# Performance work log

Measured on AMD Instinct MI355X. Metric: run time of the kernel, lower is better.

The kernel has to match this reference:

```python
import jax, jax.numpy as jnp
import numpy as np
from jax import lax

NEG = -1e30  # log-space 'zero' that stays finite for stable grads

T, B, V, L = 2000, 64, 128, 100


def ctc_cost(acts, labels2d, sizes, label_lens):
    """warp-ctc style CTC: acts are raw logits (T,B,V), blank index 0.
    Returns summed negative log-likelihood over the batch, shape (1,)."""
    Tn, Bn, Vn = acts.shape
    Ln = labels2d.shape[1]
    S = 2 * Ln + 1  # extended label length: blank,l1,blank,l2,...,blank
    lp = jax.nn.log_softmax(acts, axis=-1)  # (T,B,V)

    # extended label sequence per example: even positions blank(0), odd = labels
    ext = jnp.zeros((Bn, S), dtype=labels2d.dtype).at[:, 1::2].set(labels2d)
    # skip (s-2 -> s) allowed iff ext[s] != blank and ext[s] != ext[s-2]
    prev2 = jnp.concatenate([jnp.full((Bn, 2), -1, ext.dtype), ext[:, :-2]], axis=1)
    can_skip = (ext != 0) & (ext != prev2)  # (B,S)

    # gather per-state emission log-probs for all timesteps: (T,B,S)
    lp_ext = jnp.take_along_axis(lp, jnp.broadcast_to(ext[None], (Tn, Bn, S)), axis=2)

    # alpha init at t=0: states 0 (blank) and 1 (first label)
    alpha0 = (jnp.full((Bn, S), NEG, lp.dtype)
              .at[:, 0].set(lp_ext[0, :, 0])
              .at[:, 1].set(lp_ext[0, :, 1]))

    # per-timestep activity mask: freeze alpha once t >= sizes[b]
    active = jnp.arange(1, Tn)[:, None] < sizes[None, :]  # (T-1, B)

    def step(alpha, x):
        lp_t, act = x  # (B,S), (B,)
        a1 = jnp.concatenate([jnp.full((Bn, 1), NEG, alpha.dtype), alpha[:, :-1]], axis=1)
        a2 = jnp.concatenate([jnp.full((Bn, 2), NEG, alpha.dtype), alpha[:, :-2]], axis=1)
        a2 = jnp.where(can_skip, a2, NEG)
        new = jnp.logaddexp(jnp.logaddexp(alpha, a1), a2) + lp_t
        alpha = jnp.where(act[:, None], new, alpha)
        return alpha, None

    alpha, _ = lax.scan(step, alpha0, (lp_ext[1:], active))

    # log-likelihood ends at extended states S_b-1 (final blank) and S_b-2 (final label)
    S_b = 2 * label_lens + 1
    last = jnp.take_along_axis(alpha, (S_b - 1)[:, None], axis=1)[:, 0]
    last2 = jnp.take_along_axis(alpha, (S_b - 2)[:, None], axis=1)[:, 0]
    ll = jnp.logaddexp(last, last2)  # (B,)
    return -jnp.sum(ll)[None]  # shape (1,) like the torch module


def setup_inputs() -> dict:
    key = jax.random.key(0)
    k1, k2, k3 = jax.random.split(key, 3)
    inp = jax.random.normal(k1, (T, B, V), dtype=jnp.float32)
    # labels in [1, V): 0 is reserved for blank
    target = jax.random.randint(k2, (B * L,), 1, V, dtype=jnp.int32)
    # frame counts in [T//2, T], always >= 2L+1 so every path is feasible
    sizes = jax.random.randint(k3, (B,), T // 2, T + 1, dtype=jnp.int32)
    label_lens = jnp.full((B,), L, dtype=jnp.int32)
    return {"input": inp, "target": target, "sizes": sizes, "label_lens": label_lens}


def reference(input, target, sizes, label_lens):
    labels2d = target.reshape(sizes.shape[0], -1)  # all label_lens equal -> clean reshape
    return ctc_cost(input, labels2d, sizes, label_lens)
```

## Files before the change

kernel.cpp:

```cpp
#include <hip/hip_runtime.h>


#define TT 2000
#define BB 64
#define VV 128
#define LL 100
#define REC 104
#define REC_BASE 256
#define NEGF (-1e30f)
#define L2E 1.44269504f
#define LN2 0.69314718f

#define SB_STATE (REC_BASE + BB * TT * REC)
#define AREA 336

__device__ __forceinline__ float wave_max64(float v) {
#pragma unroll
  for (int o = 32; o > 0; o >>= 1) v = fmaxf(v, __shfl_xor(v, o, 64));
  return v;
}
__device__ __forceinline__ float wave_sum64(float v) {
#pragma unroll
  for (int o = 32; o > 0; o >>= 1) v += __shfl_xor(v, o, 64);
  return v;
}

__global__ __launch_bounds__(256) void k_gather(const float* __restrict__ acts,
                                                const int* __restrict__ target,
                                                float* __restrict__ ws) {
  const int lane = threadIdx.x & 63;
  const int w = threadIdx.x >> 6;
  const int r = blockIdx.x * 4 + w;
  if (r >= TT * BB) return;
  const int b = r % BB;
  const int t = r / BB;
  const float* row = acts + (size_t)r * VV;
  float x0 = row[lane];
  float x1 = row[lane + 64];
  float m = wave_max64(fmaxf(x0, x1));
  float e = __builtin_exp2f((x0 - m) * L2E) + __builtin_exp2f((x1 - m) * L2E);
  float s = wave_sum64(e);
  float lse = m + __builtin_log2f(s) * LN2;
  const int* lab = target + b * LL;
  int c1 = lab[lane];
  int j2 = 64 + lane;
  int c2 = (j2 < LL) ? lab[j2] : 1;
  float y1lo = __shfl(x0, c1 & 63, 64);
  float y1hi = __shfl(x1, c1 & 63, 64);
  float y1 = (c1 < 64) ? y1lo : y1hi;
  float y2lo = __shfl(x0, c2 & 63, 64);
  float y2hi = __shfl(x1, c2 & 63, 64);
  float y2 = (c2 < 64) ? y2lo : y2hi;
  float g1 = y1 - lse;
  float g2 = (j2 < LL) ? (y2 - lse) : NEGF;
  float gb = __shfl(x0, 0, 64) - lse;
  float gm = wave_max64(fmaxf(fmaxf(g1, g2), gb));
  float q1 = __builtin_exp2f((g1 - gm) * L2E);
  float q2 = (j2 < LL) ? __builtin_exp2f((g2 - gm) * L2E) : 0.0f;
  float* rec = ws + REC_BASE + ((size_t)b * TT + t) * REC;
  rec[2 + lane] = q1;
  if (lane < 38) rec[66 + lane] = q2;
  if (lane == 0) { rec[0] = __builtin_exp2f((gb - gm) * L2E); rec[1] = gm; }
}

#define BPER __builtin_amdgcn_ds_bpermute

#define DECLR(P) float2 P##h0, P##h1, P##h2, P##h3; \
                 float4 P##q0, P##q1, P##q2, P##q3; float P##aY

#define PREF(P, bidx) do {                                                   \
  int bi_ = (bidx); bi_ = (bi_ < bcap) ? bi_ : bcap; if (bi_ < 0) bi_ = 0;   \
  const float* r0_ = recs_b + (size_t)(tA + TS * 4 * bi_) * REC;             \
  P##h0 = *(const float2*)(r0_);                                             \
  P##h1 = *(const float2*)(r0_ + TS * REC);                                  \
  P##h2 = *(const float2*)(r0_ + TS * 2 * REC);                              \
  P##h3 = *(const float2*)(r0_ + TS * 3 * REC);                              \
  float2 lo0_ = *(const float2*)(r0_ + vofs);                                \
  float2 hi0_ = *(const float2*)(r0_ + vofs + 2);                            \
  float2 lo1_ = *(const float2*)(r0_ + TS * REC + vofs);                     \
  float2 hi1_ = *(const float2*)(r0_ + TS * REC + vofs + 2);                 \
  float2 lo2_ = *(const float2*)(r0_ + TS * 2 * REC + vofs);                 \
  float2 hi2_ = *(const float2*)(r0_ + TS * 2 * REC + vofs + 2);             \
  float2 lo3_ = *(const float2*)(r0_ + TS * 3 * REC + vofs);                 \
  float2 hi3_ = *(const float2*)(r0_ + TS * 3 * REC + vofs + 2);             \
  P##aY = r0_[ayofs];                                                        \
  if constexpr (DIR) {                                                       \
    P##q0 = (float4){hi0_.y, hi0_.x, lo0_.y * cmask, lo0_.x * cmask};        \
    P##q1 = (float4){hi1_.y, hi1_.x, lo1_.y * cmask, lo1_.x * cmask};        \
    P##q2 = (float4){hi2_.y, hi2_.x, lo2_.y * cmask, lo2_.x * cmask};        \
    P##q3 = (float4){hi3_.y, hi3_.x, lo3_.y * cmask, lo3_.x * cmask};        \
  } else {                                                                   \
    P##q0 = (float4){lo0_.x, lo0_.y, hi0_.x, hi0_.y};                        \
    P##q1 = (float4){lo1_.x, lo1_.y, hi1_.x, hi1_.y};                        \
    P##q2 = (float4){lo2_.x, lo2_.y, hi2_.x, hi2_.y};                        \
    P##q3 = (float4){lo3_.x, lo3_.y, hi3_.x, hi3_.y};                        \
  }                                                                          \
} while (0)

#define STEP(qbv, gmv, cx, cy, bx, by, ay, NH) do {                          \
  const float qb_ = (qbv); msum += (gmv);                                    \
  o3 = __builtin_fmaf(cs_o3, o1, o3 + o2) * (cy);                            \
  o2 = (o2 + o1) * qb_;                                                      \
  o1 = __builtin_fmaf(cs_o1, h1, o1 + o0) * (cx);                            \
  o0 = (o0 + h1) * qb_;                                                      \
  if (NH >= 1) { h1 = __builtin_fmaf(cs_h1, h3, h1 + h2) * (by);             \
                 h2 = (h2 + h3) * qb_; }                                     \
  if (NH >= 2) { h3 = __builtin_fmaf(cs_h3, h5, h3 + h4) * (bx);             \
                 h4 = (h4 + h5) * qb_; }                                     \
  if (NH >= 3) { h5 = __builtin_fmaf(cs_h5, h7, h5 + h6) * (ay);             \
                 h6 = (h6 + h7) * qb_; }                                     \
} while (0)

#define COMPA(P) do {                                                        \
  STEP(P##h0.x, P##h0.y, P##q0.z, P##q0.w, P##q0.x, P##q0.y, P##aY, 3);      \
  STEP(P##h1.x, P##h1.y, P##q1.z, P##q1.w, P##q1.x, P##q1.y, 0.f, 2);        \
  STEP(P##h2.x, P##h2.y, P##q2.z, P##q2.w, P##q2.x, P##q2.y, 0.f, 1);        \
  STEP(P##h3.x, P##h3.y, P##q3.z, P##q3.w, 0.f, 0.f, 0.f, 0);                \
  *(float4*)(exb + 4 * l) = (float4){o0, o1, o2, o3};                        \
  ((int*)exb)[256 + l] = offs;                                               \
} while (0)

#define FINL() do {                                                          \
  asm volatile("" ::: "memory");                                             \
  float4 L1_ = *(const float4*)(exb + 4 * ((l >= 1) ? (l - 1) : 0));         \
  float4 L2_ = *(const float4*)(exb + 4 * ((l >= 2) ? (l - 2) : 0));         \
  int ro1_ = ((const int*)exb)[256 + ((l >= 1) ? (l - 1) : 0)];              \
  int ro2_ = ((const int*)exb)[256 + ((l >= 2) ? (l - 2) : 0)];              \
  ro1_ = (l >= 1) ? ro1_ : -(1 << 29);                                       \
  ro2_ = (l >= 2) ? ro2_ : -(1 << 29);                                       \
  float m_ = fmaxf(fmaxf(o0, o1), fmaxf(o2, o3));                            \
  int eb_ = (int)((__float_as_uint(m_) >> 23) & 255u);                       \
  int t1_ = offs + (eb_ ? (eb_ - 127) : -126);                               \
  int mx_ = (ro1_ > ro2_) ? ro1_ : ro2_;                                     \
  int onew_ = (t1_ > mx_) ? t1_ : mx_;                                       \
  int ds_ = offs - onew_;  ds_ = (ds_ < -300) ? -300 : ds_;                  \
  int d1_ = ro1_ - onew_, d2_ = ro2_ - onew_;                                \
  d1_ = (d1_ < -300) ? -300 : d1_;                                           \
  d2_ = (d2_ < -300) ? -300 : d2_;                                           \
  o0 = ldexpf(o0, ds_); o1 = ldexpf(o1, ds_);                                \
  o2 = ldexpf(o2, ds_); o3 = ldexpf(o3, ds_);                                \
  h1 = ldexpf(L1_.w, d1_) * msk1;                                            \
  h2 = ldexpf(L1_.z, d1_) * msk2;                                            \
  h3 = ldexpf(L1_.y, d1_) * msk3;                                            \
  h4 = ldexpf(L1_.x, d1_) * msk4;                                            \
  h5 = ldexpf(L2_.w, d2_) * msk5;                                            \
  h6 = ldexpf(L2_.z, d2_) * msk6;                                            \
  h7 = ldexpf(L2_.y, d2_) * msk7;                                            \
  offs = onew_;                                                              \
} while (0)

template <int DIR>
__device__ __forceinline__ void run_chain(const int* __restrict__ target,
                                          const int* __restrict__ lablens,
                                          const float* __restrict__ recs_b,
                                          float* exb, int size, int b, int l,
                                          float* __restrict__ ws) {
  const int mid = (size - 1) >> 1;
  const int sizeP = DIR ? (size - 1 - mid) : (mid + 1);
  const int* lab = target + b * LL;
  const int lc = (l < 50) ? l : 50;
  const int vofs = DIR ? (100 - 2 * lc) : (2 * lc);
  const int tA = DIR ? (size - 2) : 1;
  constexpr int TS = DIR ? -1 : 1;
  const int bcap = DIR ? ((size - 5) >> 2) : 498;
  int ay_ = DIR ? (104 - 2 * l) : (2 * l - 1);
  ay_ = (ay_ < 0) ? 0 : ((ay_ > 103) ? 103 : ay_);
  const int ayofs = ay_;
  const float cmask = (l < 50) ? 1.f : 0.f;
  const int idx1 = ((l + 63) & 63) << 2;
  const float msk1 = (4 * l - 1 >= 0) ? 1.f : 0.f;
  const float msk2 = (4 * l - 2 >= 0) ? 1.f : 0.f;
  const float msk3 = (4 * l - 3 >= 0) ? 1.f : 0.f;
  const float msk4 = (4 * l - 4 >= 0) ? 1.f : 0.f;
  const float msk5 = (4 * l - 5 >= 0) ? 1.f : 0.f;
  const float msk6 = (4 * l - 6 >= 0) ? 1.f : 0.f;
  const float msk7 = (4 * l - 7 >= 0) ? 1.f : 0.f;
  int i0, i1, i2, i3, i4, i5;
  if constexpr (DIR == 0) { i0 = 2*l+1; i1 = 2*l; i2 = 2*l-1; i3 = 2*l-2; i4 = 2*l-3; i5 = 2*l-4; }
  else { i0 = 98-2*l; i1 = 99-2*l; i2 = 100-2*l; i3 = 101-2*l; i4 = 102-2*l; i5 = 103-2*l; }
#define CLM(x) ((x) < 0 ? 0 : ((x) > 99 ? 99 : (x)))
  const int La = lab[CLM(i0)], Lb_ = lab[CLM(i1)], Lc = lab[CLM(i2)];
  const int Ld = lab[CLM(i3)], Le = lab[CLM(i4)], Lf = lab[CLM(i5)];
  const float cs_o3 = (La != Lb_) ? 1.f : 0.f;
  const float cs_o1 = (Lb_ != Lc) ? 1.f : 0.f;
  const float cs_h1 = (Lc != Ld) ? 1.f : 0.f;
  const float cs_h3 = (Ld != Le) ? 1.f : 0.f;
  const float cs_h5 = (Le != Lf) ? 1.f : 0.f;
  float o0 = 0.f, o1 = 0.f, o2 = 0.f, o3 = 0.f;
  float h1 = 0.f, h2 = 0.f, h3 = 0.f, h4 = 0.f, h5 = 0.f, h6 = 0.f, h7 = 0.f;
  int offs = 0;
  float msum;
  if constexpr (DIR == 0) {
    msum = recs_b[1];
    if (l == 0) { o0 = recs_b[0]; o1 = recs_b[2]; }
    if (l == 1) { h3 = recs_b[2]; h4 = recs_b[0]; }
    if (l == 2) { h7 = recs_b[2]; }
  } else {
    const float* recL = recs_b + (size_t)(size - 1) * REC;
    msum = recL[1];
    const int Lbv = lablens[b];
    const int r0v = 200 - 2 * Lbv;
    auto gi = [&](int rho) -> float {
      if (rho != r0v && rho != r0v + 1) return 0.f;
      if ((rho & 1) == 0) return recL[0];
      return recL[2 + 99 - ((rho - 1) >> 1)];
    };
    o0 = gi(4*l); o1 = gi(4*l+1); o2 = gi(4*l+2); o3 = gi(4*l+3);
    h1 = gi(4*l-1); h2 = gi(4*l-2); h3 = gi(4*l-3); h4 = gi(4*l-4);
    h5 = gi(4*l-5); h6 = gi(4*l-6); h7 = gi(4*l-7);
  }

  const int nb = (sizeP - 1) >> 2;
  DECLR(A); DECLR(B); DECLR(C); DECLR(D);
  PREF(A, 0); PREF(B, 1); PREF(C, 2);
  int blk = 0;
  for (; blk + 4 <= nb; blk += 4) {
    COMPA(A); PREF(D, blk + 3); FINL();
    COMPA(B); PREF(A, blk + 4); FINL();
    COMPA(C); PREF(B, blk + 5); FINL();
    COMPA(D); PREF(C, blk + 6); FINL();
  }
  if (nb - blk >= 1) { COMPA(A); FINL(); }
  if (nb - blk >= 2) { COMPA(B); FINL(); }
  if (nb - blk >= 3) { COMPA(C); FINL(); }
  {
    int rno1 = BPER(idx1, offs);
    int dtl = rno1 - offs;
    dtl = (dtl > 120) ? 120 : ((dtl < -300) ? -300 : dtl);
    for (int tau = 1 + 4 * nb; tau < sizeP; ++tau) {
      const float* rt = recs_b + (size_t)(DIR ? (size - 1 - tau) : tau) * REC;
      float2 hh = *(const float2*)rt;
      float cx, cy;
      if constexpr (DIR == 0) {
        float2 qc = *(const float2*)(rt + 2 + 2 * lc);
        cx = qc.x; cy = qc.y;
      } else {
        float2 qc = *(const float2*)(rt + vofs + 2);
        cx = qc.y * cmask; cy = qc.x * cmask;
      }
      int rp = BPER(idx1, __float_as_int(o3));
      float p = ldexpf(__int_as_float(rp), dtl) * msk1;
      msum += hh.y;
      o3 = __builtin_fmaf(cs_o3, o1, o3 + o2) * cy;
      o2 = (o2 + o1) * hh.x;
      o1 = __builtin_fmaf(cs_o1, p, o1 + o0) * cx;
      o0 = (o0 + p) * hh.x;
    }
    if constexpr (DIR == 0) {
      int rp = BPER(idx1, __float_as_int(o3));
      float p = ldexpf(__int_as_float(rp), dtl) * msk1;
      o3 = __builtin_fmaf(cs_o3, o1, o3 + o2);
      o2 = o2 + o1;
      o1 = __builtin_fmaf(cs_o1, p, o1 + o0);
      o0 = o0 + p;
    }
  }
  float* da = ws + SB_STATE + (size_t)(2 * b + DIR) * AREA;
  ((float4*)da)[l] = (float4){o0, o1, o2, o3};
  ((int*)da)[256 + l] = offs;
  if (l == 0) da[320] = msum;
}

__global__ __launch_bounds__(128, 1) void k_alpha(const int* __restrict__ target,
                                                  const int* __restrict__ sizes,
                                                  const int* __restrict__ lablens,
                                                  float* __restrict__ ws) {
  __shared__ float ldsA[2 * 384];
  const int b = blockIdx.x;
  const int dirw = threadIdx.x >> 6;
  const int l = threadIdx.x & 63;
  float* exb = ldsA + dirw * 384;
  const int size = sizes[b];
  const float* recs_b = ws + REC_BASE + (size_t)b * TT * REC;
  if (dirw == 0) run_chain<0>(target, lablens, recs_b, exb, size, b, l, ws);
  else           run_chain<1>(target, lablens, recs_b, exb, size, b, l, ws);
}

__global__ __launch_bounds__(64) void k_comb(float* __restrict__ ws) {
  const int b = blockIdx.x;
  const int l = threadIdx.x;
  const float* fa = ws + SB_STATE + (size_t)(2 * b) * AREA;
  const float* ba = fa + AREA;
  float4 av = ((const float4*)fa)[l];
  int eF = ((const int*)fa)[256 + l];
  float msF = fa[320], msB = ba[320];
  float pr0, pr1, pr2, pr3; int ex0, ex1, ex2, ex3, sb0, sb1, sb2, sb3;
#define CMP(k, AV, PR, EX, SBE) do {                                         \
    int s_ = 4 * l + (k);                                                    \
    int rho_ = 200 - s_;                                                     \
    int rc_ = (rho_ < 0) ? 0 : rho_;                                         \
    float g_ = ba[rc_];                                                      \
    int eB_ = ((const int*)ba)[256 + (rc_ >> 2)];                            \
    float p_ = (AV) * g_;                                                    \
    bool ok_ = (rho_ >= 0) && (p_ > 0.f);                                    \
    int eb_ = (int)((__float_as_uint(p_) >> 23) & 255u);                     \
    SBE = eF + eB_;                                                          \
    EX = ok_ ? (SBE + (eb_ ? eb_ - 127 : -140)) : (int)0xC0000000;           \
    PR = ok_ ? p_ : 0.f;                                                     \
  } while (0)
  CMP(0, av.x, pr0, ex0, sb0);
  CMP(1, av.y, pr1, ex1, sb1);
  CMP(2, av.z, pr2, ex2, sb2);
  CMP(3, av.w, pr3, ex3, sb3);
  int Em = ex0 > ex1 ? ex0 : ex1;
  Em = ex2 > Em ? ex2 : Em;
  Em = ex3 > Em ? ex3 : Em;
#pragma unroll
  for (int o = 32; o > 0; o >>= 1) {
    int t = __shfl_xor(Em, o, 64);
    Em = (t > Em) ? t : Em;
  }
  float v = 0.f;
#define ACC(PR, SBE) do { if (PR > 0.f) {                                    \
    int sh_ = SBE - Em; sh_ = sh_ < -300 ? -300 : (sh_ > 300 ? 300 : sh_);   \
    v += ldexpf(PR, sh_); } } while (0)
  ACC(pr0, sb0); ACC(pr1, sb1); ACC(pr2, sb2); ACC(pr3, sb3);
  float S = wave_sum64(v);
  if (l == 0) ws[b] = msF + msB + LN2 * ((float)Em + __builtin_log2f(S));
}

__global__ __launch_bounds__(64) void k_final(const float* __restrict__ ws, float* __restrict__ out) {
  float v = (threadIdx.x < BB) ? ws[threadIdx.x] : 0.0f;
  v = wave_sum64(v);
  if (threadIdx.x == 0) out[0] = -v;
}

extern "C" void kernel_launch(void* const* d_in, const int* in_sizes, int n_in,
                              void* d_out, int out_size, void* d_ws, size_t ws_size,
                              hipStream_t stream) {
  const float* acts  = (const float*)d_in[0];
  const int* target  = (const int*)d_in[1];
  const int* sizes   = (const int*)d_in[2];
  const int* lablens = (const int*)d_in[3];
  float* ws  = (float*)d_ws;
  float* out = (float*)d_out;
  const int nrec = TT * BB;
  k_gather<<<dim3(nrec / 4), dim3(256), 0, stream>>>(acts, target, ws);
  k_alpha<<<dim3(BB), dim3(128), 0, stream>>>(target, sizes, lablens, ws);
  k_comb<<<dim3(BB), dim3(64), 0, stream>>>(ws);
  k_final<<<dim3(1), dim3(64), 0, stream>>>(ws, out);
}
```

Before: 131.2 us.

## Store per-step emission ratios as packed bf16 and shorten the prefetch pipeline

The gather kernel now writes the per-label emission ratios as round-to-nearest bf16 pairs packed into 32-bit words, which shrinks each record from 104 to 56 floats. The alpha chain loads one packed word per timestep for its two states and unpacks with shifts and masks. This cuts workspace traffic in both the gather write and the latency-bound recurrence reads. The software prefetch ring also drops from four buffered blocks to three, trading prefetch depth for fewer live registers. The risk is lost precision in the CTC likelihood, since bf16 emission factors are multiplied over up to 2000 steps.

Result: faster. 124.5 us (-5.1%).

```diff
diff --git a/kernel.cpp b/kernel.cpp
--- a/kernel.cpp
+++ b/kernel.cpp
@@ -5,13 +5,13 @@
 #define BB 64
 #define VV 128
 #define LL 100
-#define REC 104
+#define RECW 56
 #define REC_BASE 256
 #define NEGF (-1e30f)
 #define L2E 1.44269504f
 #define LN2 0.69314718f
 
-#define SB_STATE (REC_BASE + BB * TT * REC)
+#define SB_STATE (REC_BASE + BB * TT * RECW)
 #define AREA 336
 
 __device__ __forceinline__ float wave_max64(float v) {
@@ -23,6 +23,12 @@
 #pragma unroll
   for (int o = 32; o > 0; o >>= 1) v += __shfl_xor(v, o, 64);
   return v;
+}
+__device__ __forceinline__ float blo(unsigned u) { return __uint_as_float(u << 16); }
+__device__ __forceinline__ float bhi(unsigned u) { return __uint_as_float(u & 0xFFFF0000u); }
+__device__ __forceinline__ unsigned b16(float x) {
+  unsigned b = __float_as_uint(x);
+  return (b + 0x7FFFu + ((b >> 16) & 1u)) >> 16;
 }
 
 __global__ __launch_bounds__(256) void k_gather(const float* __restrict__ acts,
@@ -42,59 +48,52 @@
   float s = wave_sum64(e);
   float lse = m + __builtin_log2f(s) * LN2;
   const int* lab = target + b * LL;
-  int c1 = lab[lane];
-  int j2 = 64 + lane;
-  int c2 = (j2 < LL) ? lab[j2] : 1;
-  float y1lo = __shfl(x0, c1 & 63, 64);
-  float y1hi = __shfl(x1, c1 & 63, 64);
-  float y1 = (c1 < 64) ? y1lo : y1hi;
-  float y2lo = __shfl(x0, c2 & 63, 64);
-  float y2hi = __shfl(x1, c2 & 63, 64);
-  float y2 = (c2 < 64) ? y2lo : y2hi;
-  float g1 = y1 - lse;
-  float g2 = (j2 < LL) ? (y2 - lse) : NEGF;
+  const int j = lane;
+  int ilo = (2 * j < 100) ? 2 * j : 99;
+  int ihi = (2 * j + 1 < 100) ? 2 * j + 1 : 99;
+  int cl = lab[ilo], ch = lab[ihi];
+  float ya = __shfl(x0, cl & 63, 64), yb = __shfl(x1, cl & 63, 64);
+  float ylo = (cl < 64) ? ya : yb;
+  float yc = __shfl(x0, ch & 63, 64), yd = __shfl(x1, ch & 63, 64);
+  float yhi = (ch < 64) ? yc : yd;
+  float glo = (j < 50) ? (ylo - lse) : NEGF;
+  float ghi = (j < 50) ? (yhi - lse) : NEGF;
   float gb = __shfl(x0, 0, 64) - lse;
-  float gm = wave_max64(fmaxf(fmaxf(g1, g2), gb));
-  float q1 = __builtin_exp2f((g1 - gm) * L2E);
-  float q2 = (j2 < LL) ? __builtin_exp2f((g2 - gm) * L2E) : 0.0f;
-  float* rec = ws + REC_BASE + ((size_t)b * TT + t) * REC;
-  rec[2 + lane] = q1;
-  if (lane < 38) rec[66 + lane] = q2;
-  if (lane == 0) { rec[0] = __builtin_exp2f((gb - gm) * L2E); rec[1] = gm; }
+  float gm = wave_max64(fmaxf(fmaxf(glo, ghi), gb));
+  float qlo = __builtin_exp2f((glo - gm) * L2E);
+  float qhi = __builtin_exp2f((ghi - gm) * L2E);
+  unsigned u = b16(qlo) | (b16(qhi) << 16);
+  unsigned* rec = (unsigned*)(ws + REC_BASE + ((size_t)b * TT + t) * RECW);
+  if (j < 50) rec[2 + j] = u;
+  if (j == 50) rec[52] = 0u;
+  if (j == 0) {
+    ((float*)rec)[0] = __builtin_exp2f((gb - gm) * L2E);
+    ((float*)rec)[1] = gm;
+  }
 }
 
 #define BPER __builtin_amdgcn_ds_bpermute
+#define CL50(x) ((x) < 0 ? 0 : ((x) > 50 ? 50 : (x)))
 
 #define DECLR(P) float2 P##h0, P##h1, P##h2, P##h3; \
-                 float4 P##q0, P##q1, P##q2, P##q3; float P##aY
+                 unsigned P##b0, P##b1, P##b2, P##b3, P##c0, P##c1, P##c2, P##c3, P##uA
 
 #define PREF(P, bidx) do {                                                   \
   int bi_ = (bidx); bi_ = (bi_ < bcap) ? bi_ : bcap; if (bi_ < 0) bi_ = 0;   \
-  const float* r0_ = recs_b + (size_t)(tA + TS * 4 * bi_) * REC;             \
+  const float* r0_ = recs_b + (size_t)(tA + TS * 4 * bi_) * RECW;            \
   P##h0 = *(const float2*)(r0_);                                             \
-  P##h1 = *(const float2*)(r0_ + TS * REC);                                  \
-  P##h2 = *(const float2*)(r0_ + TS * 2 * REC);                              \
-  P##h3 = *(const float2*)(r0_ + TS * 3 * REC);                              \
-  float2 lo0_ = *(const float2*)(r0_ + vofs);                                \
-  float2 hi0_ = *(const float2*)(r0_ + vofs + 2);                            \
-  float2 lo1_ = *(const float2*)(r0_ + TS * REC + vofs);                     \
-  float2 hi1_ = *(const float2*)(r0_ + TS * REC + vofs + 2);                 \
-  float2 lo2_ = *(const float2*)(r0_ + TS * 2 * REC + vofs);                 \
-  float2 hi2_ = *(const float2*)(r0_ + TS * 2 * REC + vofs + 2);             \
-  float2 lo3_ = *(const float2*)(r0_ + TS * 3 * REC + vofs);                 \
-  float2 hi3_ = *(const float2*)(r0_ + TS * 3 * REC + vofs + 2);             \
-  P##aY = r0_[ayofs];                                                        \
-  if constexpr (DIR) {                                                       \
-    P##q0 = (float4){hi0_.y, hi0_.x, lo0_.y * cmask, lo0_.x * cmask};        \
-    P##q1 = (float4){hi1_.y, hi1_.x, lo1_.y * cmask, lo1_.x * cmask};        \
-    P##q2 = (float4){hi2_.y, hi2_.x, lo2_.y * cmask, lo2_.x * cmask};        \
-    P##q3 = (float4){hi3_.y, hi3_.x, lo3_.y * cmask, lo3_.x * cmask};        \
-  } else {                                                                   \
-    P##q0 = (float4){lo0_.x, lo0_.y, hi0_.x, hi0_.y};                        \
-    P##q1 = (float4){lo1_.x, lo1_.y, hi1_.x, hi1_.y};                        \
-    P##q2 = (float4){lo2_.x, lo2_.y, hi2_.x, hi2_.y};                        \
-    P##q3 = (float4){lo3_.x, lo3_.y, hi3_.x, hi3_.y};                        \
-  }                                                                          \
+  P##h1 = *(const float2*)(r0_ + TS * RECW);                                 \
+  P##h2 = *(const float2*)(r0_ + TS * 2 * RECW);                             \
+  P##h3 = *(const float2*)(r0_ + TS * 3 * RECW);                             \
+  P##b0 = ((const unsigned*)r0_)[pbofs];                                     \
+  P##c0 = ((const unsigned*)r0_)[pcofs];                                     \
+  P##b1 = ((const unsigned*)(r0_ + TS * RECW))[pbofs];                       \
+  P##c1 = ((const unsigned*)(r0_ + TS * RECW))[pcofs];                       \
+  P##b2 = ((const unsigned*)(r0_ + TS * 2 * RECW))[pbofs];                   \
+  P##c2 = ((const unsigned*)(r0_ + TS * 2 * RECW))[pcofs];                   \
+  P##b3 = ((const unsigned*)(r0_ + TS * 3 * RECW))[pbofs];                   \
+  P##c3 = ((const unsigned*)(r0_ + TS * 3 * RECW))[pcofs];                   \
+  P##uA = ((const unsigned*)r0_)[payofs];                                    \
 } while (0)
 
 #define STEP(qbv, gmv, cx, cy, bx, by, ay, NH) do {                          \
@@ -111,11 +110,22 @@
                  h6 = (h6 + h7) * qb_; }                                     \
 } while (0)
 
+#define UQ(P, K, QV) float4 QV; do {                                         \
+  if constexpr (DIR) {                                                       \
+    QV = (float4){bhi(P##b##K), blo(P##b##K),                                \
+                  bhi(P##c##K) * cmask, blo(P##c##K) * cmask};               \
+  } else {                                                                   \
+    QV = (float4){blo(P##b##K), bhi(P##b##K), blo(P##c##K), bhi(P##c##K)};   \
+  }                                                                          \
+} while (0)
+
 #define COMPA(P) do {                                                        \
-  STEP(P##h0.x, P##h0.y, P##q0.z, P##q0.w, P##q0.x, P##q0.y, P##aY, 3);      \
-  STEP(P##h1.x, P##h1.y, P##q1.z, P##q1.w, P##q1.x, P##q1.y, 0.f, 2);        \
-  STEP(P##h2.x, P##h2.y, P##q2.z, P##q2.w, P##q2.x, P##q2.y, 0.f, 1);        \
-  STEP(P##h3.x, P##h3.y, P##q3.z, P##q3.w, 0.f, 0.f, 0.f, 0);                \
+  UQ(P, 0, q0_); UQ(P, 1, q1_); UQ(P, 2, q2_); UQ(P, 3, q3_);                \
+  float aYv = DIR ? blo(P##uA) : bhi(P##uA);                                 \
+  STEP(P##h0.x, P##h0.y, q0_.z, q0_.w, q0_.x, q0_.y, aYv, 3);                \
+  STEP(P##h1.x, P##h1.y, q1_.z, q1_.w, q1_.x, q1_.y, 0.f, 2);                \
+  STEP(P##h2.x, P##h2.y, q2_.z, q2_.w, q2_.x, q2_.y, 0.f, 1);                \
+  STEP(P##h3.x, P##h3.y, q3_.z, q3_.w, 0.f, 0.f, 0.f, 0);                    \
   *(float4*)(exb + 4 * l) = (float4){o0, o1, o2, o3};                        \
   ((int*)exb)[256 + l] = offs;                                               \
 } while (0)
@@ -159,13 +169,12 @@
   const int sizeP = DIR ? (size - 1 - mid) : (mid + 1);
   const int* lab = target + b * LL;
   const int lc = (l < 50) ? l : 50;
-  const int vofs = DIR ? (100 - 2 * lc) : (2 * lc);
   const int tA = DIR ? (size - 2) : 1;
   constexpr int TS = DIR ? -1 : 1;
   const int bcap = DIR ? ((size - 5) >> 2) : 498;
-  int ay_ = DIR ? (104 - 2 * l) : (2 * l - 1);
-  ay_ = (ay_ < 0) ? 0 : ((ay_ > 103) ? 103 : ay_);
-  const int ayofs = ay_;
+  const int pbofs = 2 + (DIR ? CL50(50 - l) : CL50(l - 1));
+  const int pcofs = 2 + (DIR ? CL50(49 - l) : CL50(l));
+  const int payofs = 2 + (DIR ? CL50(51 - l) : CL50(l - 2));
   const float cmask = (l < 50) ? 1.f : 0.f;
   const int idx1 = ((l + 63) & 63) << 2;
   const float msk1 = (4 * l - 1 >= 0) ? 1.f : 0.f;
@@ -192,18 +201,21 @@
   float msum;
   if constexpr (DIR == 0) {
     msum = recs_b[1];
-    if (l == 0) { o0 = recs_b[0]; o1 = recs_b[2]; }
-    if (l == 1) { h3 = recs_b[2]; h4 = recs_b[0]; }
-    if (l == 2) { h7 = recs_b[2]; }
+    float q0i = blo(((const unsigned*)recs_b)[2]);
+    if (l == 0) { o0 = recs_b[0]; o1 = q0i; }
+    if (l == 1) { h3 = q0i; h4 = recs_b[0]; }
+    if (l == 2) { h7 = q0i; }
   } else {
-    const float* recL = recs_b + (size_t)(size - 1) * REC;
+    const float* recL = recs_b + (size_t)(size - 1) * RECW;
     msum = recL[1];
     const int Lbv = lablens[b];
     const int r0v = 200 - 2 * Lbv;
     auto gi = [&](int rho) -> float {
       if (rho != r0v && rho != r0v + 1) return 0.f;
       if ((rho & 1) == 0) return recL[0];
-      return recL[2 + 99 - ((rho - 1) >> 1)];
+      int mm = 99 - ((rho - 1) >> 1);
+      unsigned u = ((const unsigned*)recL)[2 + (mm >> 1)];
+      return (mm & 1) ? bhi(u) : blo(u);
     };
     o0 = gi(4*l); o1 = gi(4*l+1); o2 = gi(4*l+2); o3 = gi(4*l+3);
     h1 = gi(4*l-1); h2 = gi(4*l-2); h3 = gi(4*l-3); h4 = gi(4*l-4);
@@ -211,32 +223,30 @@
   }
 
   const int nb = (sizeP - 1) >> 2;
-  DECLR(A); DECLR(B); DECLR(C); DECLR(D);
-  PREF(A, 0); PREF(B, 1); PREF(C, 2);
+  DECLR(A); DECLR(B); DECLR(C);
+  PREF(A, 0); PREF(B, 1);
   int blk = 0;
-  for (; blk + 4 <= nb; blk += 4) {
-    COMPA(A); PREF(D, blk + 3); FINL();
-    COMPA(B); PREF(A, blk + 4); FINL();
-    COMPA(C); PREF(B, blk + 5); FINL();
-    COMPA(D); PREF(C, blk + 6); FINL();
+  for (; blk + 3 <= nb; blk += 3) {
+    COMPA(A); PREF(C, blk + 2); FINL();
+    COMPA(B); PREF(A, blk + 3); FINL();
+    COMPA(C); PREF(B, blk + 4); FINL();
   }
   if (nb - blk >= 1) { COMPA(A); FINL(); }
   if (nb - blk >= 2) { COMPA(B); FINL(); }
-  if (nb - blk >= 3) { COMPA(C); FINL(); }
   {
     int rno1 = BPER(idx1, offs);
     int dtl = rno1 - offs;
     dtl = (dtl > 120) ? 120 : ((dtl < -300) ? -300 : dtl);
     for (int tau = 1 + 4 * nb; tau < sizeP; ++tau) {
-      const float* rt = recs_b + (size_t)(DIR ? (size - 1 - tau) : tau) * REC;
+      const float* rt = recs_b + (size_t)(DIR ? (size - 1 - tau) : tau) * RECW;
       float2 hh = *(const float2*)rt;
       float cx, cy;
       if constexpr (DIR == 0) {
-        float2 qc = *(const float2*)(rt + 2 + 2 * lc);
-        cx = qc.x; cy = qc.y;
+        unsigned u = ((const unsigned*)rt)[2 + lc];
+        cx = blo(u); cy = bhi(u);
       } else {
-        float2 qc = *(const float2*)(rt + vofs + 2);
-        cx = qc.y * cmask; cy = qc.x * cmask;
+        unsigned u = ((const unsigned*)rt)[2 + CL50(50 - l)];
+        cx = bhi(u) * cmask; cy = blo(u) * cmask;
       }
       int rp = BPER(idx1, __float_as_int(o3));
       float p = ldexpf(__int_as_float(rp), dtl) * msk1;
@@ -271,7 +281,7 @@
   const int l = threadIdx.x & 63;
   float* exb = ldsA + dirw * 384;
   const int size = sizes[b];
-  const float* recs_b = ws + REC_BASE + (size_t)b * TT * REC;
+  const float* recs_b = ws + REC_BASE + (size_t)b * TT * RECW;
   if (dirw == 0) run_chain<0>(target, lablens, recs_b, exb, size, b, l, ws);
   else           run_chain<1>(target, lablens, recs_b, exb, size, b, l, ws);
 }
```
